# Kernel optimization log

Measured on AMD Instinct MI355X. Metric: run time of the kernel, lower is better.

Reference implementation:

```python
import jax, jax.numpy as jnp
import numpy as np

K = 5       # local window size (odd)
G = 4       # groups

def _gconv1x1(x, w):
    # grouped 1x1 conv: x (b,c,h,w), w (g, c_out_g, c_in_g) -> (b,g,c_out_g,h,w)
    b, c, h, wd = x.shape
    g, co, ci = w.shape
    xg = x.reshape(b, g, ci, h, wd)
    return jnp.einsum('bgihw,goi->bgohw', xg, w)

def _windows(f, h, w):
    # f: (b,g,n,h+2p,w+2p) -> (b,g,n,h,w,K*K), row-major over (ki,kj)
    # matches torch .unfold(2,K,1).unfold(3,K,1).view(..., -1)
    return jnp.stack([f[..., i:i + h, j:j + w]
                      for i in range(K) for j in range(K)], axis=-1)

def setup_inputs() -> dict:
    key = jax.random.key(0)
    k1, k2, k3, k4 = jax.random.split(key, 4)
    x = jax.random.normal(k1, (2, 128, 96, 96), dtype=jnp.float32)
    wq = jax.random.normal(k2, (G, 32, 32), dtype=jnp.float32) * 0.1
    wk = jax.random.normal(k3, (G, 32, 32), dtype=jnp.float32) * 0.1
    wv = jax.random.normal(k4, (G, 32, 32), dtype=jnp.float32) * 0.1
    return {"x": x, "wq": wq, "wk": wk, "wv": wv}

def reference(x, wq, wk, wv):
    b, c, h, w = x.shape
    p = K // 2
    # query: plain grouped 1x1 conv, broadcast over window dim
    q = _gconv1x1(x, wq)[..., None]                      # (b,g,n,h,w,1)
    # key/value: reflect-pad (1x1 conv commutes with padding, same as torch's
    # Conv2d(..., padding=k//2, padding_mode='reflect'))
    xp = jnp.pad(x, ((0, 0), (0, 0), (p, p), (p, p)), mode='reflect')
    kf = _gconv1x1(xp, wk)                               # (b,g,n,h+2p,w+2p)
    vf = _gconv1x1(xp, wv)
    kwin = _windows(kf, h, w)                            # (b,g,n,h,w,K*K)
    vwin = _windows(vf, h, w)
    attn = jax.nn.softmax(q * kwin, axis=-1)             # per-channel window softmax
    y = (attn * vwin).sum(-1)                            # (b,g,n,h,w)
    return y.reshape(b, -1, h, w)                        # (b, c_out, h, w)
```

## Files before the change

kernel.cpp:

```cpp
#include <hip/hip_runtime.h>


#define HW 96
#define RG 12
#define NPOS 144

__device__ __forceinline__ int refl(int i) {
    i = (i < 0) ? -i : i;
    i = (i > 95) ? (190 - i) : i;
    return i;
}

__global__ __launch_bounds__(256) void fused_attn(
    const float* __restrict__ x, const float* __restrict__ wq,
    const float* __restrict__ wk, const float* __restrict__ wv,
    float* __restrict__ out)
{
    __shared__ float xs[32 * NPOS + 64];
    __shared__ float kb[32 * NPOS];
    __shared__ float vb[32 * NPOS];

    const int tid  = threadIdx.x;
    const int tile = blockIdx.x;
    const int g    = blockIdx.y;
    const int b    = blockIdx.z;
    const int h0 = (tile / 12) * 8;
    const int w0 = (tile % 12) * 8;

    const float* xg = x + (size_t)(b * 128 + g * 32) * (HW * HW);

    for (int idx = tid; idx < 32 * NPOS; idx += 256) {
        int pos = idx % NPOS;
        int ch  = idx / NPOS;
        int iy = refl(h0 + pos / RG - 2);
        int ix = refl(w0 + pos % RG - 2);
        xs[idx] = xg[ch * (HW * HW) + iy * HW + ix];
    }
    __syncthreads();

    const int wid  = tid >> 6;
    const int lane = tid & 63;
    const int n0   = __builtin_amdgcn_readfirstlane(wid * 8);
    const float* wkp = wk + (g * 32 + n0) * 32;
    const float* wvp = wv + (g * 32 + n0) * 32;
    const float* wqp = wq + (g * 32 + n0) * 32;

    {
        float ak0[8], ak1[8], ak2[8], av0[8], av1[8], av2[8];
        #pragma unroll
        for (int n = 0; n < 8; n++) { ak0[n]=ak1[n]=ak2[n]=0.f; av0[n]=av1[n]=av2[n]=0.f; }
        #pragma unroll 4
        for (int i = 0; i < 32; i++) {
            float x0 = xs[i * NPOS + lane];
            float x1 = xs[i * NPOS + 64 + lane];
            float x2 = xs[i * NPOS + 128 + lane];
            #pragma unroll
            for (int n = 0; n < 8; n++) {
                float a = wkp[n * 32 + i];
                float c = wvp[n * 32 + i];
                ak0[n] += a * x0; ak1[n] += a * x1; ak2[n] += a * x2;
                av0[n] += c * x0; av1[n] += c * x1; av2[n] += c * x2;
            }
        }
        #pragma unroll
        for (int n = 0; n < 8; n++) {
            kb[(n0 + n) * NPOS + lane]      = ak0[n];
            vb[(n0 + n) * NPOS + lane]      = av0[n];
            kb[(n0 + n) * NPOS + 64 + lane] = ak1[n];
            vb[(n0 + n) * NPOS + 64 + lane] = av1[n];
            if (lane < 16) {
                kb[(n0 + n) * NPOS + 128 + lane] = ak2[n];
                vb[(n0 + n) * NPOS + 128 + lane] = av2[n];
            }
        }
    }
    __syncthreads();

    const int ty = lane >> 3, tx = lane & 7;
    const int center = (ty + 2) * RG + (tx + 2);

    float qacc[8];
    #pragma unroll
    for (int n = 0; n < 8; n++) qacc[n] = 0.f;
    #pragma unroll 4
    for (int i = 0; i < 32; i++) {
        float xi = xs[i * NPOS + center];
        #pragma unroll
        for (int n = 0; n < 8; n++) qacc[n] += wqp[n * 32 + i] * xi;
    }

    float* outp = out + (size_t)((b * 128 + g * 32 + n0) * HW + (h0 + ty)) * HW + (w0 + tx);
    for (int n = 0; n < 8; n++) {
        const float* kbn = kb + (n0 + n) * NPOS;
        const float* vbn = vb + (n0 + n) * NPOS;
        float q = qacc[n];
        float s[25];
        float m = -3.4e38f;
        #pragma unroll
        for (int t = 0; t < 25; t++) {
            int dy = t / 5, dx = t % 5;
            s[t] = q * kbn[(ty + dy) * RG + tx + dx];
            m = fmaxf(m, s[t]);
        }
        float den = 0.f, num = 0.f;
        #pragma unroll
        for (int t = 0; t < 25; t++) {
            int dy = t / 5, dx = t % 5;
            float e = __expf(s[t] - m);
            den += e;
            num += e * vbn[(ty + dy) * RG + tx + dx];
        }
        outp[n * (HW * HW)] = num / den;
    }
}

extern "C" void kernel_launch(void* const* d_in, const int* in_sizes, int n_in,
                              void* d_out, int out_size, void* d_ws, size_t ws_size,
                              hipStream_t stream) {
    const float* x  = (const float*)d_in[0];
    const float* wq = (const float*)d_in[1];
    const float* wk = (const float*)d_in[2];
    const float* wv = (const float*)d_in[3];
    float* out = (float*)d_out;

    dim3 grid(144, 4, 2);
    fused_attn<<<grid, 256, 0, stream>>>(x, wq, wk, wv, out);
}
```

Before: 110.6 us.

## Alias K buffer onto input tile, fuse Q projection, drop softmax max pass

Reuses the staged input buffer for the key results so shared memory per block shrinks, adding a barrier before the keys are written. The query projection is computed in the same loop as the key/value projections. The softmax no longer subtracts the running max and uses a hardware reciprocal, removing one pass over the window. This is less numerically robust for large logits and may raise register pressure.

```diff
diff --git a/kernel.cpp b/kernel.cpp
--- a/kernel.cpp
+++ b/kernel.cpp
@@ -16,9 +16,10 @@
     const float* __restrict__ wk, const float* __restrict__ wv,
     float* __restrict__ out)
 {
-    __shared__ float xs[32 * NPOS + 64];
-    __shared__ float kb[32 * NPOS];
-    __shared__ float vb[32 * NPOS];
+    __shared__ float smem[4672 + 4608];
+    float* const xs = smem;
+    float* const kb = smem;
+    float* const vb = smem + 4672;
 
     const int tid  = threadIdx.x;
     const int tile = blockIdx.x;
@@ -45,72 +46,60 @@
     const float* wvp = wv + (g * 32 + n0) * 32;
     const float* wqp = wq + (g * 32 + n0) * 32;
 
-    {
-        float ak0[8], ak1[8], ak2[8], av0[8], av1[8], av2[8];
-        #pragma unroll
-        for (int n = 0; n < 8; n++) { ak0[n]=ak1[n]=ak2[n]=0.f; av0[n]=av1[n]=av2[n]=0.f; }
-        #pragma unroll 4
-        for (int i = 0; i < 32; i++) {
-            float x0 = xs[i * NPOS + lane];
-            float x1 = xs[i * NPOS + 64 + lane];
-            float x2 = xs[i * NPOS + 128 + lane];
-            #pragma unroll
-            for (int n = 0; n < 8; n++) {
-                float a = wkp[n * 32 + i];
-                float c = wvp[n * 32 + i];
-                ak0[n] += a * x0; ak1[n] += a * x1; ak2[n] += a * x2;
-                av0[n] += c * x0; av1[n] += c * x1; av2[n] += c * x2;
-            }
-        }
+    const int ty = lane >> 3, tx = lane & 7;
+    const int center = (ty + 2) * RG + (tx + 2);
+
+    float qacc[8];
+    float ak0[8], ak1[8], ak2[8], av0[8], av1[8], av2[8];
+    #pragma unroll
+    for (int n = 0; n < 8; n++) {
+        qacc[n] = 0.f;
+        ak0[n]=ak1[n]=ak2[n]=0.f; av0[n]=av1[n]=av2[n]=0.f;
+    }
+    #pragma unroll 4
+    for (int i = 0; i < 32; i++) {
+        float xq = xs[i * NPOS + center];
+        float x0 = xs[i * NPOS + lane];
+        float x1 = xs[i * NPOS + 64 + lane];
+        float x2 = xs[i * NPOS + 128 + lane];
         #pragma unroll
         for (int n = 0; n < 8; n++) {
-            kb[(n0 + n) * NPOS + lane]      = ak0[n];
-            vb[(n0 + n) * NPOS + lane]      = av0[n];
-            kb[(n0 + n) * NPOS + 64 + lane] = ak1[n];
-            vb[(n0 + n) * NPOS + 64 + lane] = av1[n];
-            if (lane < 16) {
-                kb[(n0 + n) * NPOS + 128 + lane] = ak2[n];
-                vb[(n0 + n) * NPOS + 128 + lane] = av2[n];
-            }
+            float a = wkp[n * 32 + i];
+            float c = wvp[n * 32 + i];
+            qacc[n] += wqp[n * 32 + i] * xq;
+            ak0[n] += a * x0; ak1[n] += a * x1; ak2[n] += a * x2;
+            av0[n] += c * x0; av1[n] += c * x1; av2[n] += c * x2;
         }
     }
     __syncthreads();
 
-    const int ty = lane >> 3, tx = lane & 7;
-    const int center = (ty + 2) * RG + (tx + 2);
-
-    float qacc[8];
     #pragma unroll
-    for (int n = 0; n < 8; n++) qacc[n] = 0.f;
-    #pragma unroll 4
-    for (int i = 0; i < 32; i++) {
-        float xi = xs[i * NPOS + center];
-        #pragma unroll
-        for (int n = 0; n < 8; n++) qacc[n] += wqp[n * 32 + i] * xi;
+    for (int n = 0; n < 8; n++) {
+        kb[(n0 + n) * NPOS + lane]      = ak0[n];
+        vb[(n0 + n) * NPOS + lane]      = av0[n];
+        kb[(n0 + n) * NPOS + 64 + lane] = ak1[n];
+        vb[(n0 + n) * NPOS + 64 + lane] = av1[n];
+        if (lane < 16) {
+            kb[(n0 + n) * NPOS + 128 + lane] = ak2[n];
+            vb[(n0 + n) * NPOS + 128 + lane] = av2[n];
+        }
     }
+    __syncthreads();
 
     float* outp = out + (size_t)((b * 128 + g * 32 + n0) * HW + (h0 + ty)) * HW + (w0 + tx);
     for (int n = 0; n < 8; n++) {
         const float* kbn = kb + (n0 + n) * NPOS;
         const float* vbn = vb + (n0 + n) * NPOS;
         float q = qacc[n];
-        float s[25];
-        float m = -3.4e38f;
-        #pragma unroll
-        for (int t = 0; t < 25; t++) {
-            int dy = t / 5, dx = t % 5;
-            s[t] = q * kbn[(ty + dy) * RG + tx + dx];
-            m = fmaxf(m, s[t]);
-        }
         float den = 0.f, num = 0.f;
         #pragma unroll
         for (int t = 0; t < 25; t++) {
             int dy = t / 5, dx = t % 5;
-            float e = __expf(s[t] - m);
+            float e = __expf(q * kbn[(ty + dy) * RG + tx + dx]);
             den += e;
             num += e * vbn[(ty + dy) * RG + tx + dx];
         }
-        outp[n * (HW * HW)] = num / den;
+        outp[n * (HW * HW)] = num * __builtin_amdgcn_rcpf(den);
     }
 }
 
```

Result: faster. 104.0 us (-5.9%).
